# Optimization experiments

Measured on AMD Instinct MI355X. Metric: run time of the kernel, lower is better.

The kernel has to match this reference:

```python
import jax, jax.numpy as jnp
import numpy as np

VOCAB, EMBED, HIDDEN, NUM_CLASSES = 32000, 512, 1024, 10
PAD_IDX = 0


def setup_inputs() -> dict:
    key = jax.random.key(0)
    ks = jax.random.split(key, 8)
    x = jax.random.randint(ks[0], (64, 512), 0, VOCAB, dtype=jnp.int32)
    emb = jax.random.uniform(ks[1], (VOCAB, EMBED), jnp.float32, -0.1, 0.1)
    emb = emb.at[PAD_IDX].set(0.0)
    def xavier(k, shape):
        fan_out, fan_in = shape
        lim = jnp.sqrt(6.0 / (fan_in + fan_out)).astype(jnp.float32)
        return jax.random.uniform(k, shape, jnp.float32, -lim, lim)
    # layer 0: input EMBED+HIDDEN -> 4*HIDDEN; layer 1: 2*HIDDEN -> 4*HIDDEN
    W0 = xavier(ks[2], (4 * HIDDEN, EMBED + HIDDEN))
    W1 = xavier(ks[3], (4 * HIDDEN, 2 * HIDDEN))
    # bias: forget-gate chunk initialized to 1.0 (chunk order: i, f, g, o)
    b = jnp.zeros((4 * HIDDEN,), jnp.float32).at[HIDDEN:2 * HIDDEN].set(1.0)
    V = xavier(ks[4], (NUM_CLASSES, HIDDEN))
    bV = jnp.zeros((NUM_CLASSES,), jnp.float32)
    return {"x": x, "emb": emb, "W0": W0, "b0": b, "W1": W1, "b1": b, "V": V, "bV": bV}


def _cell(x_in, h, c, W, b):
    # gates: [B, 4H] = cat(x_in, h) @ W.T + b
    gates = jnp.concatenate([x_in, h], axis=-1) @ W.T + b
    i, f, g, o = jnp.split(gates, 4, axis=-1)
    c_new = jax.nn.sigmoid(f) * c + jax.nn.sigmoid(i) * jnp.tanh(g)
    h_new = jax.nn.sigmoid(o) * jnp.tanh(c_new)
    return h_new, c_new


def reference(x, emb, W0, b0, W1, b1, V, bV):
    B, T = x.shape
    embedded = emb[x]                       # [B, T, E]
    xs = jnp.swapaxes(embedded, 0, 1)       # [T, B, E]
    Ws, bs = (W0, W1), (b0, b1)
    h0 = jnp.zeros((2, B, HIDDEN), embedded.dtype)
    c0 = jnp.zeros((2, B, HIDDEN), embedded.dtype)

    def step(carry, x_t):
        h, c = carry
        layer_in = x_t
        hs, cs = [], []
        for i in range(2):
            h_new, c_new = _cell(layer_in, h[i], c[i], Ws[i], bs[i])
            hs.append(h_new)
            cs.append(c_new)
            layer_in = h_new
        return (jnp.stack(hs), jnp.stack(cs)), None

    (h_final, _), _ = jax.lax.scan(step, (h0, c0), xs)
    return h_final[-1] @ V.T + bV           # [B, NUM_CLASSES]
```

## Files before the change

### kernel.cpp

```cpp
#include <hip/hip_runtime.h>
#include <stdint.h>


typedef __attribute__((ext_vector_type(8))) short bf16x8;
typedef __attribute__((ext_vector_type(4))) float f32x4;

__device__ __forceinline__ unsigned short f2bf(float x) {
    unsigned u = __float_as_uint(x);
    u = (u + 0x7FFFu + ((u >> 16) & 1u)) >> 16;
    return (unsigned short)u;
}

__device__ __forceinline__ f32x4 mfma16(bf16x8 a, bf16x8 b, f32x4 c) {
    return __builtin_amdgcn_mfma_f32_16x16x32_bf16(a, b, c, 0, 0, 0);
}

__device__ __forceinline__ bf16x8 ldh(const unsigned short* p) {
    union { unsigned long long q[2]; bf16x8 v; } u;
    unsigned long long* a = (unsigned long long*)p;
    u.q[0] = __hip_atomic_load(a + 0, __ATOMIC_RELAXED, __HIP_MEMORY_SCOPE_AGENT);
    u.q[1] = __hip_atomic_load(a + 1, __ATOMIC_RELAXED, __HIP_MEMORY_SCOPE_AGENT);
    return u.v;
}

__device__ __forceinline__ void poll64(const unsigned int* base, int lane,
                                       unsigned target) {
    const unsigned int* p = base + lane;
    for (;;) {
        unsigned a = __hip_atomic_load(p, __ATOMIC_RELAXED, __HIP_MEMORY_SCOPE_AGENT);
        if (__all((int)(a >= target))) break;
        __builtin_amdgcn_s_sleep(2);
    }
}

__device__ __forceinline__ void poll128(const unsigned int* base, int lane,
                                        unsigned target) {
    const unsigned int* p0 = base + lane;
    const unsigned int* p1 = base + 64 + lane;
    for (;;) {
        unsigned a = __hip_atomic_load(p0, __ATOMIC_RELAXED, __HIP_MEMORY_SCOPE_AGENT);
        unsigned b = __hip_atomic_load(p1, __ATOMIC_RELAXED, __HIP_MEMORY_SCOPE_AGENT);
        if (__all((int)((a >= target) && (b >= target)))) break;
        __builtin_amdgcn_s_sleep(2);
    }
}

__device__ __forceinline__ float fsigm(float x) {
    x = fminf(fmaxf(x, -60.f), 60.f);
    return __builtin_amdgcn_rcpf(1.f + __expf(-x));
}
__device__ __forceinline__ float ftanh(float x) {
    x = fminf(fmaxf(x, -15.f), 15.f);
    float e = __expf(-2.f * x);
    return (1.f - e) * __builtin_amdgcn_rcpf(1.f + e);
}

__global__ __launch_bounds__(256) void embed_kernel(
    const int* __restrict__ x, const float* __restrict__ emb,
    unsigned short* __restrict__ xs)
{
    int e = blockIdx.x * 256 + threadIdx.x;
    int t  = e >> 12;
    int r  = e & 4095;
    int b  = r >> 6;
    int k8 = (r & 63) << 3;
    int tok = x[b * 512 + t];
    const float* src = emb + (size_t)tok * 512 + k8;
    unsigned short* dst = xs + ((size_t)(t * 64 + b)) * 512 + k8;
#pragma unroll
    for (int i = 0; i < 8; ++i) dst[i] = f2bf(src[i]);
}

__global__ __launch_bounds__(256) void init_kernel(unsigned int* __restrict__ p, int n)
{
    int i = blockIdx.x * 256 + threadIdx.x;
    if (i < n) p[i] = 0u;
}

#define LDS_GWS_OFF 131072
#define GWS_TILE    272
#define LDS_TOTAL   148480
#define RELIDX      2048
#define RING_MASK   127
#define SLOT_USH    65536
#define NBANK       16

__global__ __launch_bounds__(512) void lstm_kernel_df(
    const unsigned short* __restrict__ xs,
    unsigned short* __restrict__ h0ring,
    unsigned short* __restrict__ h1ring,
    float* __restrict__ h1f,
    unsigned int* __restrict__ bar,
    const float* __restrict__ W0, const float* __restrict__ b0,
    const float* __restrict__ W1, const float* __restrict__ b1)
{
    extern __shared__ char smem[];
    bf16x8* Afrag = (bf16x8*)smem;
    float*  gws   = (float*)(smem + LDS_GWS_OFF);

    const int wg  = blockIdx.x;
    const int tid = threadIdx.x;
    const bool isL1 = (wg >= 128);
    const int rr  = wg & 127;
    const int g   = rr >> 6;
    const int w   = rr & 63;
    const int w16 = w * 16;
    const float* W = isL1 ? W1 : W0;
    const int wstride = isL1 ? 2048 : 1536;
    const float* bias = isL1 ? b1 : b0;
    const unsigned int* bk = bar + (wg & (NBANK - 1)) * 256;

    for (int f = tid; f < 8192; f += 512) {
        int laneE = f & 63;
        int gt    = (f >> 6) & 3;
        int kb    = f >> 8;
        int m16   = laneE & 15;
        int q     = laneE >> 4;
        int c     = m16 >> 2;
        int s     = m16 & 3;
        int grow  = c * 1024 + w16 + gt * 4 + s;
        const float* src = W + (size_t)grow * wstride + kb * 32 + q * 8;
        bf16x8 v;
#pragma unroll
        for (int i = 0; i < 8; ++i) v[i] = (short)f2bf(src[i]);
        Afrag[f] = v;
    }

    const int lane = tid & 63;
    const int wid  = tid >> 6;
    const int bt   = wid & 1;
    const int ksh  = wid >> 1;
    const int n16  = lane & 15;
    const int q4   = lane >> 4;
    const int row  = g * 32 + bt * 16 + n16;
    const int nkreg = isL1 ? 8 : 4;

    bf16x8 rf[8][4];
    {
        int m16 = lane & 15;
        int q   = lane >> 4;
        int c   = m16 >> 2;
        int s   = m16 & 3;
#pragma unroll
        for (int jr = 0; jr < 8; ++jr) {
            if (jr < nkreg) {
                int kb = 32 + ksh + 4 * jr;
#pragma unroll
                for (int gt = 0; gt < 4; ++gt) {
                    int grow = c * 1024 + w16 + gt * 4 + s;
                    const float* src = W + (size_t)grow * wstride + kb * 32 + q * 8;
                    bf16x8 v;
#pragma unroll
                    for (int i = 0; i < 8; ++i) v[i] = (short)f2bf(src[i]);
                    rf[jr][gt] = v;
                }
            }
        }
    }

    const int eb   = tid >> 4;
    const int ecol = tid & 15;
    const int ebt  = tid >> 8;
    const int en   = eb & 15;
    const int egt  = ecol >> 2;
    const int es   = ecol & 3;
    const int erow = g * 32 + eb;
    float bi[4];
#pragma unroll
    for (int c = 0; c < 4; ++c) bi[c] = bias[c * 1024 + w16 + ecol];
    float cst = 0.f;
    const float* gs0 = gws + (size_t)((ebt * 2 + 0) * 4 + egt) * GWS_TILE + es * 17 + en;
    const float* gs1 = gws + (size_t)((ebt * 2 + 1) * 4 + egt) * GWS_TILE + es * 17 + en;
    float* gwr = gws + (size_t)((bt * 2 + (ksh & 1)) * 4) * GWS_TILE + q4 * 68 + n16;

    __syncthreads();

    f32x4 acc[4];
#pragma unroll
    for (int i = 0; i < 4; ++i) acc[i] = (f32x4){0.f, 0.f, 0.f, 0.f};

    if (!isL1) {
        const unsigned short* xsp = xs + ((size_t)row) * 512 + q4 * 8;
#pragma unroll
        for (int j = 0; j < 4; ++j) {
            int kb = ksh + 4 * j;
            bf16x8 bf = *(const bf16x8*)(xsp + kb * 32);
#pragma unroll
            for (int gt = 0; gt < 4; ++gt)
                acc[gt] = mfma16(Afrag[(kb * 4 + gt) * 64 + lane], bf, acc[gt]);
        }
    }

    for (int tick = 0; tick < 513; ++tick) {
        if (tick > 0) {
            unsigned target = (unsigned)tick;
            if ((tick & RING_MASK) == 0) {
                if (wid == 0)      poll128(bk,       lane, target);
                else if (wid == 4) poll128(bk + 128, lane, target);
                __syncthreads();
                if (wid == 0)
                    __builtin_amdgcn_fence(__ATOMIC_ACQUIRE, "agent");
                __syncthreads();
            } else {
                if (wid == 0)              poll64(bk + g * 64, lane, target);
                else if (isL1 && wid == 4) poll64(bk + 128 + g * 64, lane, target);
                __syncthreads();
            }
        }

        int t = isL1 ? (tick - 1) : tick;
        if (t >= 0 && t < 512) {
            if (!isL1) {
                if (t > 0) {
                    const unsigned short* hp =
                        h0ring + (size_t)((t - 1) & RING_MASK) * SLOT_USH
                               + (size_t)row * 1024 + q4 * 8;
#pragma unroll
                    for (int j = 4; j < 8; ++j) {
                        int kb = ksh + 4 * j;
                        bf16x8 bf = *(const bf16x8*)(hp + (kb - 16) * 32);
#pragma unroll
                        for (int gt = 0; gt < 4; ++gt)
                            acc[gt] = mfma16(Afrag[(kb * 4 + gt) * 64 + lane], bf, acc[gt]);
                    }
#pragma unroll
                    for (int j = 0; j < 4; ++j) {
                        int kb = 32 + ksh + 4 * j;
                        bf16x8 bf = *(const bf16x8*)(hp + (kb - 16) * 32);
#pragma unroll
                        for (int gt = 0; gt < 4; ++gt)
                            acc[gt] = mfma16(rf[j][gt], bf, acc[gt]);
                    }
                }
            } else {
                const unsigned short* hp0 =
                    h0ring + (size_t)(t & RING_MASK) * SLOT_USH
                           + (size_t)row * 1024 + q4 * 8;
#pragma unroll
                for (int j = 0; j < 8; ++j) {
                    int kb = ksh + 4 * j;
                    bf16x8 bf = *(const bf16x8*)(hp0 + kb * 32);
#pragma unroll
                    for (int gt = 0; gt < 4; ++gt)
                        acc[gt] = mfma16(Afrag[(kb * 4 + gt) * 64 + lane], bf, acc[gt]);
                }
                if (t > 0) {
                    const unsigned short* hp1 =
                        h1ring + (size_t)((t - 1) & RING_MASK) * SLOT_USH
                               + (size_t)row * 1024 + q4 * 8;
#pragma unroll
                    for (int j = 0; j < 8; ++j) {
                        int kb = ksh + 4 * j;
                        bf16x8 bf = *(const bf16x8*)(hp1 + kb * 32);
#pragma unroll
                        for (int gt = 0; gt < 4; ++gt)
                            acc[gt] = mfma16(rf[j][gt], bf, acc[gt]);
                    }
                }
            }

            if (ksh < 2) {
#pragma unroll
                for (int gt = 0; gt < 4; ++gt)
#pragma unroll
                    for (int r2 = 0; r2 < 4; ++r2)
                        gwr[gt * GWS_TILE + r2 * 17] = acc[gt][r2];
            }
            __syncthreads();
            if (ksh >= 2) {
#pragma unroll
                for (int gt = 0; gt < 4; ++gt)
#pragma unroll
                    for (int r2 = 0; r2 < 4; ++r2)
                        gwr[gt * GWS_TILE + r2 * 17] += acc[gt][r2];
            }
            __syncthreads();

            float xi = gs0[0]   + gs1[0]   + bi[0];
            float xf = gs0[68]  + gs1[68]  + bi[1];
            float xg = gs0[136] + gs1[136] + bi[2];
            float xo = gs0[204] + gs1[204] + bi[3];
            float si = fsigm(xi);
            float sf = fsigm(xf);
            float tg = ftanh(xg);
            float so = fsigm(xo);
            float cn = sf * cst + si * tg;
            cst = cn;
            float h  = so * ftanh(cn);
            unsigned hb  = (unsigned)f2bf(h);
            unsigned hup = (unsigned)__shfl_down((int)hb, 1);
            if (!(tid & 1)) {
                unsigned hv = hb | (hup << 16);
                unsigned short* hw =
                    (isL1 ? h1ring : h0ring) + (size_t)(t & RING_MASK) * SLOT_USH;
                unsigned int* hp32 =
                    (unsigned int*)(hw + (size_t)erow * 1024 + w16 + ecol);
                __hip_atomic_store(hp32, hv, __ATOMIC_RELAXED, __HIP_MEMORY_SCOPE_AGENT);
            }
            if (isL1 && t == 511)
                h1f[(size_t)erow * 1024 + w16 + ecol] = h;
            __syncthreads();
        }

        if (tick < 512) {
            if (tid < NBANK) {
                __hip_atomic_store(bar + tid * 256 + (isL1 ? 128 : 0) + g * 64 + w,
                                   (unsigned)(tick + 1),
                                   __ATOMIC_RELAXED, __HIP_MEMORY_SCOPE_AGENT);
            }
#pragma unroll
            for (int i = 0; i < 4; ++i) acc[i] = (f32x4){0.f, 0.f, 0.f, 0.f};
            int tn = tick + 1;
            if (!isL1 && tn < 512) {
                const unsigned short* xsp =
                    xs + ((size_t)(tn * 64 + row)) * 512 + q4 * 8;
#pragma unroll
                for (int j = 0; j < 4; ++j) {
                    int kb = ksh + 4 * j;
                    bf16x8 bf = *(const bf16x8*)(xsp + kb * 32);
#pragma unroll
                    for (int gt = 0; gt < 4; ++gt)
                        acc[gt] = mfma16(Afrag[(kb * 4 + gt) * 64 + lane], bf, acc[gt]);
                }
            }
        }
    }
}

__global__ __launch_bounds__(512) void lstm_kernel_fb(
    const unsigned short* __restrict__ xs,
    unsigned short* __restrict__ h0buf,
    unsigned short* __restrict__ h1buf,
    float* __restrict__ h1f,
    unsigned int* __restrict__ bar,
    const float* __restrict__ W0, const float* __restrict__ b0,
    const float* __restrict__ W1, const float* __restrict__ b1)
{
    extern __shared__ char smem[];
    bf16x8* Afrag = (bf16x8*)smem;
    float*  gws   = (float*)(smem + LDS_GWS_OFF);

    const int wg  = blockIdx.x;
    const int tid = threadIdx.x;
    const bool isL1 = (wg >= 128);
    const int w   = isL1 ? wg - 128 : wg;
    const int w8  = w * 8;
    const int nk  = isL1 ? 64 : 48;
    const float* W = isL1 ? W1 : W0;
    const int wstride = isL1 ? 2048 : 1536;
    const float* bias = isL1 ? b1 : b0;

    for (int f = tid; f < nk * 128; f += 512) {
        int kblk = f >> 7;
        int r    = f & 127;
        int mt   = r >> 6;
        int lane = r & 63;
        int m16  = lane & 15;
        int q    = lane >> 4;
        int c    = m16 >> 2;
        int ul   = mt * 4 + (m16 & 3);
        int grow = c * 1024 + w8 + ul;
        const float* src = W + (size_t)grow * wstride + kblk * 32 + q * 8;
        bf16x8 v;
#pragma unroll
        for (int i = 0; i < 8; ++i) v[i] = (short)f2bf(src[i]);
        Afrag[f] = v;
    }

    const int lane = tid & 63;
    const int wid  = tid >> 6;
    const int wv   = wid & 3;
    const int kh   = tid >> 8;
    const int n16  = lane & 15;
    const int q4   = lane >> 4;
    const int brow = wv * 16 + n16;

    float bi[2][4];
#pragma unroll
    for (int cell = 0; cell < 2; ++cell) {
        int j = w8 + q4 * 2 + cell;
#pragma unroll
        for (int c = 0; c < 4; ++c) bi[cell][c] = bias[c * 1024 + j];
    }
    float cst0 = 0.f, cst1 = 0.f;

    __syncthreads();

    f32x4 acc0 = (f32x4){0.f, 0.f, 0.f, 0.f};
    f32x4 acc1 = (f32x4){0.f, 0.f, 0.f, 0.f};

    if (!isL1) {
        const unsigned short* xsp = xs + ((size_t)brow) * 512 + q4 * 8;
        int k0 = kh ? 8 : 0;
#pragma unroll
        for (int kb2 = 0; kb2 < 8; ++kb2) {
            int kb = k0 + kb2;
            bf16x8 bf = *(const bf16x8*)(xsp + kb * 32);
            acc0 = mfma16(Afrag[(kb * 2 + 0) * 64 + lane], bf, acc0);
            acc1 = mfma16(Afrag[(kb * 2 + 1) * 64 + lane], bf, acc1);
        }
    }

    for (int tick = 0; tick < 513; ++tick) {
        if (tick > 0) {
            unsigned target = (unsigned)tick;
            if (wg == 0) {
                if (tid < 256) {
                    while (__hip_atomic_load(&bar[tid * 8], __ATOMIC_RELAXED,
                                             __HIP_MEMORY_SCOPE_AGENT) < target)
                        __builtin_amdgcn_s_sleep(1);
                }
                __syncthreads();
                if (tid < 8)
                    __hip_atomic_store(&bar[RELIDX + tid * 32], target,
                                       __ATOMIC_RELAXED, __HIP_MEMORY_SCOPE_AGENT);
            } else {
                if (tid == 0) {
                    while (__hip_atomic_load(&bar[RELIDX + (wg & 7) * 32],
                                             __ATOMIC_RELAXED,
                                             __HIP_MEMORY_SCOPE_AGENT) < target)
                        __builtin_amdgcn_s_sleep(1);
                }
                __syncthreads();
            }
            asm volatile("" ::: "memory");
        }

        int t = isL1 ? (tick - 1) : tick;
        if (t >= 0 && t < 512) {
            const int p = t & 1;

            if (!isL1) {
                const unsigned short* hp =
                    h0buf + (size_t)(p ^ 1) * 65536 + (size_t)brow * 1024 + q4 * 8;
                int k0 = kh ? 32 : 16;
#pragma unroll 8
                for (int kb2 = 0; kb2 < 16; ++kb2) {
                    int kb = k0 + kb2;
                    bf16x8 bf = ldh(hp + (kb - 16) * 32);
                    acc0 = mfma16(Afrag[(kb * 2 + 0) * 64 + lane], bf, acc0);
                    acc1 = mfma16(Afrag[(kb * 2 + 1) * 64 + lane], bf, acc1);
                }
            } else if (kh == 0) {
                const unsigned short* hp0 =
                    h0buf + (size_t)p * 65536 + (size_t)brow * 1024 + q4 * 8;
#pragma unroll 8
                for (int kb = 0; kb < 32; ++kb) {
                    bf16x8 bf = ldh(hp0 + kb * 32);
                    acc0 = mfma16(Afrag[(kb * 2 + 0) * 64 + lane], bf, acc0);
                    acc1 = mfma16(Afrag[(kb * 2 + 1) * 64 + lane], bf, acc1);
                }
            } else {
                const unsigned short* hp1 =
                    h1buf + (size_t)(p ^ 1) * 65536 + (size_t)brow * 1024 + q4 * 8;
#pragma unroll 8
                for (int kb = 32; kb < 64; ++kb) {
                    bf16x8 bf = ldh(hp1 + (kb - 32) * 32);
                    acc0 = mfma16(Afrag[(kb * 2 + 0) * 64 + lane], bf, acc0);
                    acc1 = mfma16(Afrag[(kb * 2 + 1) * 64 + lane], bf, acc1);
                }
            }

            float* gq = gws + wid * 512;
#pragma unroll
            for (int r = 0; r < 4; ++r) {
                gq[      q4 * 64 + r * 16 + n16] = acc0[r];
                gq[256 + q4 * 64 + r * 16 + n16] = acc1[r];
            }
            __syncthreads();

            if (kh == 0) {
                unsigned short* hw = (isL1 ? h1buf : h0buf) + (size_t)p * 65536;
                unsigned short hbits[2];
                float hflt[2];
#pragma unroll
                for (int cell = 0; cell < 2; ++cell) {
                    int ul = q4 * 2 + cell;
                    int mt = ul >> 2;
                    int r  = ul & 3;
                    const float* g0 = gws + wv * 512 + mt * 256;
                    const float* g1 = gws + (wv + 4) * 512 + mt * 256;
                    float xi = g0[0 * 64 + r * 16 + n16] + g1[0 * 64 + r * 16 + n16] + bi[cell][0];
                    float xf = g0[1 * 64 + r * 16 + n16] + g1[1 * 64 + r * 16 + n16] + bi[cell][1];
                    float xg = g0[2 * 64 + r * 16 + n16] + g1[2 * 64 + r * 16 + n16] + bi[cell][2];
                    float xo = g0[3 * 64 + r * 16 + n16] + g1[3 * 64 + r * 16 + n16] + bi[cell][3];
                    float si = fsigm(xi);
                    float sf = fsigm(xf);
                    float tg = ftanh(xg);
                    float so = fsigm(xo);
                    float cprev = cell ? cst1 : cst0;
                    float cn = sf * cprev + si * tg;
                    if (cell) cst1 = cn; else cst0 = cn;
                    float h = so * ftanh(cn);
                    hflt[cell]  = h;
                    hbits[cell] = f2bf(h);
                }
                unsigned int hv = (unsigned)hbits[0] | ((unsigned)hbits[1] << 16);
                unsigned int* hp32 =
                    (unsigned int*)(hw + (size_t)brow * 1024 + w8 + q4 * 2);
                __hip_atomic_store(hp32, hv, __ATOMIC_RELAXED, __HIP_MEMORY_SCOPE_AGENT);
                if (isL1 && t == 511) {
                    h1f[(size_t)brow * 1024 + w8 + q4 * 2 + 0] = hflt[0];
                    h1f[(size_t)brow * 1024 + w8 + q4 * 2 + 1] = hflt[1];
                }
            }
            __syncthreads();
        }

        if (tick < 512) {
            if (tid == 0) {
                asm volatile("s_waitcnt vmcnt(0)" ::: "memory");
                __hip_atomic_store(&bar[wg * 8], (unsigned)(tick + 1),
                                   __ATOMIC_RELAXED, __HIP_MEMORY_SCOPE_AGENT);
            }
            acc0 = (f32x4){0.f, 0.f, 0.f, 0.f};
            acc1 = (f32x4){0.f, 0.f, 0.f, 0.f};
            int tn = tick + 1;
            if (!isL1 && tn < 512) {
                const unsigned short* xsp =
                    xs + ((size_t)(tn * 64 + brow)) * 512 + q4 * 8;
                int k0 = kh ? 8 : 0;
#pragma unroll
                for (int kb2 = 0; kb2 < 8; ++kb2) {
                    int kb = k0 + kb2;
                    bf16x8 bf = *(const bf16x8*)(xsp + kb * 32);
                    acc0 = mfma16(Afrag[(kb * 2 + 0) * 64 + lane], bf, acc0);
                    acc1 = mfma16(Afrag[(kb * 2 + 1) * 64 + lane], bf, acc1);
                }
            }
        }
    }
}

__global__ __launch_bounds__(64) void cls_kernel(
    const float* __restrict__ h1f, const float* __restrict__ V,
    const float* __restrict__ bV, float* __restrict__ out)
{
    int b = blockIdx.x;
    int lane = threadIdx.x;
    float p[10];
#pragma unroll
    for (int c = 0; c < 10; ++c) p[c] = 0.f;
    for (int k = lane; k < 1024; k += 64) {
        float h = h1f[(size_t)b * 1024 + k];
#pragma unroll
        for (int c = 0; c < 10; ++c) p[c] += h * V[(size_t)c * 1024 + k];
    }
#pragma unroll
    for (int c = 0; c < 10; ++c) {
        float v = p[c];
#pragma unroll
        for (int off = 32; off > 0; off >>= 1) v += __shfl_down(v, off);
        if (lane == 0) out[b * 10 + c] = v + bV[c];
    }
}

extern "C" void kernel_launch(void* const* d_in, const int* in_sizes, int n_in,
                              void* d_out, int out_size, void* d_ws, size_t ws_size,
                              hipStream_t stream)
{
    const int*   x   = (const int*)d_in[0];
    const float* emb = (const float*)d_in[1];
    const float* W0  = (const float*)d_in[2];
    const float* b0  = (const float*)d_in[3];
    const float* W1  = (const float*)d_in[4];
    const float* b1  = (const float*)d_in[5];
    const float* V   = (const float*)d_in[6];
    const float* bV  = (const float*)d_in[7];
    float* out = (float*)d_out;

    char* ws = (char*)d_ws;
    unsigned short* xs = (unsigned short*)ws;

    if (ws_size >= 67387392ULL) {
        unsigned short* h0r = (unsigned short*)(ws + 33554432);
        unsigned short* h1r = (unsigned short*)(ws + 50331648);
        float*          h1f = (float*)(ws + 67108864);
        unsigned int*   bar = (unsigned int*)(ws + 67371008);

        hipLaunchKernelGGL(init_kernel, dim3(16), dim3(256), 0, stream,
                           bar, 4096);
        hipLaunchKernelGGL(embed_kernel, dim3(8192), dim3(256), 0, stream, x, emb, xs);
        hipLaunchKernelGGL(lstm_kernel_df, dim3(256), dim3(512), LDS_TOTAL, stream,
                           xs, h0r, h1r, h1f, bar, W0, b0, W1, b1);
        hipLaunchKernelGGL(cls_kernel, dim3(64), dim3(64), 0, stream, h1f, V, bV, out);
    } else {
        char* dyn = ws + 33554432;
        unsigned short* h0  = (unsigned short*)(dyn);
        unsigned short* h1  = (unsigned short*)(dyn + 262144);
        float*          h1f = (float*)(dyn + 524288);
        unsigned int*   bar = (unsigned int*)(dyn + 786432);

        hipLaunchKernelGGL(init_kernel, dim3(780), dim3(256), 0, stream,
                           (unsigned int*)dyn, 199680);
        hipLaunchKernelGGL(embed_kernel, dim3(8192), dim3(256), 0, stream, x, emb, xs);
        hipLaunchKernelGGL(lstm_kernel_fb, dim3(256), dim3(512), LDS_TOTAL, stream,
                           xs, h0, h1, h1f, bar, W0, b0, W1, b1);
        hipLaunchKernelGGL(cls_kernel, dim3(64), dim3(64), 0, stream, h1f, V, bV, out);
    }
}
```

Baseline: 3.050 ms.

## Restructure LSTM into role-split workgroups with local batch groups and partial-sum pipelines

```diff
diff --git a/kernel.cpp b/kernel.cpp
--- a/kernel.cpp
+++ b/kernel.cpp
@@ -4,102 +4,131 @@
 
 typedef __attribute__((ext_vector_type(8))) short bf16x8;
 typedef __attribute__((ext_vector_type(4))) float f32x4;
-
-__device__ __forceinline__ unsigned short f2bf(float x) {
+typedef unsigned short ush;
+typedef unsigned int u32;
+
+__device__ __forceinline__ ush f2bf(float x) {
     unsigned u = __float_as_uint(x);
     u = (u + 0x7FFFu + ((u >> 16) & 1u)) >> 16;
-    return (unsigned short)u;
+    return (ush)u;
 }
 
 __device__ __forceinline__ f32x4 mfma16(bf16x8 a, bf16x8 b, f32x4 c) {
     return __builtin_amdgcn_mfma_f32_16x16x32_bf16(a, b, c, 0, 0, 0);
 }
 
-__device__ __forceinline__ bf16x8 ldh(const unsigned short* p) {
+__device__ __forceinline__ float fsigm(float x) {
+    x = fminf(fmaxf(x, -60.f), 60.f);
+    return __builtin_amdgcn_rcpf(1.f + __expf(-x));
+}
+__device__ __forceinline__ float ftanh(float x) {
+    x = fminf(fmaxf(x, -15.f), 15.f);
+    float e = __expf(-2.f * x);
+    return (1.f - e) * __builtin_amdgcn_rcpf(1.f + e);
+}
+
+__device__ __forceinline__ u32 aload(const u32* p) {
+    return __hip_atomic_load(p, __ATOMIC_RELAXED, __HIP_MEMORY_SCOPE_AGENT);
+}
+__device__ __forceinline__ void astore(u32* p, u32 v) {
+    __hip_atomic_store(p, v, __ATOMIC_RELAXED, __HIP_MEMORY_SCOPE_AGENT);
+}
+__device__ __forceinline__ float aloadf(const float* p) {
+    return __hip_atomic_load(p, __ATOMIC_RELAXED, __HIP_MEMORY_SCOPE_AGENT);
+}
+__device__ __forceinline__ void astoref(float* p, float v) {
+    __hip_atomic_store(p, v, __ATOMIC_RELAXED, __HIP_MEMORY_SCOPE_AGENT);
+}
+__device__ __forceinline__ bf16x8 ldh(const ush* p) {
     union { unsigned long long q[2]; bf16x8 v; } u;
     unsigned long long* a = (unsigned long long*)p;
     u.q[0] = __hip_atomic_load(a + 0, __ATOMIC_RELAXED, __HIP_MEMORY_SCOPE_AGENT);
     u.q[1] = __hip_atomic_load(a + 1, __ATOMIC_RELAXED, __HIP_MEMORY_SCOPE_AGENT);
     return u.v;
 }
-
-__device__ __forceinline__ void poll64(const unsigned int* base, int lane,
-                                       unsigned target) {
-    const unsigned int* p = base + lane;
+#define WAITVM0() do { asm volatile("s_waitcnt vmcnt(0)" ::: "memory"); \
+                       __builtin_amdgcn_sched_barrier(0); } while (0)
+#define L1INV()  do { asm volatile("buffer_inv" ::: "memory"); \
+                      __builtin_amdgcn_sched_barrier(0); } while (0)
+__device__ __forceinline__ void barlg() {
+    asm volatile("s_waitcnt lgkmcnt(0)\ns_barrier" ::: "memory");
+    __builtin_amdgcn_sched_barrier(0);
+}
+
+__device__ __forceinline__ void poll64(const u32* base, int lane, unsigned target) {
+    const u32* p = base + lane;
     for (;;) {
-        unsigned a = __hip_atomic_load(p, __ATOMIC_RELAXED, __HIP_MEMORY_SCOPE_AGENT);
+        unsigned a = aload(p);
         if (__all((int)(a >= target))) break;
         __builtin_amdgcn_s_sleep(2);
     }
 }
-
-__device__ __forceinline__ void poll128(const unsigned int* base, int lane,
-                                        unsigned target) {
-    const unsigned int* p0 = base + lane;
-    const unsigned int* p1 = base + 64 + lane;
+__device__ __forceinline__ void poll128(const u32* base, int lane, unsigned target) {
+    const u32* p0 = base + lane;
+    const u32* p1 = base + 64 + lane;
     for (;;) {
-        unsigned a = __hip_atomic_load(p0, __ATOMIC_RELAXED, __HIP_MEMORY_SCOPE_AGENT);
-        unsigned b = __hip_atomic_load(p1, __ATOMIC_RELAXED, __HIP_MEMORY_SCOPE_AGENT);
+        unsigned a = aload(p0);
+        unsigned b = aload(p1);
         if (__all((int)((a >= target) && (b >= target)))) break;
         __builtin_amdgcn_s_sleep(2);
     }
 }
 
-__device__ __forceinline__ float fsigm(float x) {
-    x = fminf(fmaxf(x, -60.f), 60.f);
-    return __builtin_amdgcn_rcpf(1.f + __expf(-x));
-}
-__device__ __forceinline__ float ftanh(float x) {
-    x = fminf(fmaxf(x, -15.f), 15.f);
-    float e = __expf(-2.f * x);
-    return (1.f - e) * __builtin_amdgcn_rcpf(1.f + e);
-}
-
 __global__ __launch_bounds__(256) void embed_kernel(
     const int* __restrict__ x, const float* __restrict__ emb,
-    unsigned short* __restrict__ xs)
+    ush* __restrict__ xs)
 {
     int e = blockIdx.x * 256 + threadIdx.x;
     int t  = e >> 12;
-    int r  = e & 4095;
-    int b  = r >> 6;
-    int k8 = (r & 63) << 3;
+    int rr = e & 4095;
+    int b  = rr >> 6;
+    int k8 = (rr & 63) << 3;
     int tok = x[b * 512 + t];
     const float* src = emb + (size_t)tok * 512 + k8;
-    unsigned short* dst = xs + ((size_t)(t * 64 + b)) * 512 + k8;
+    ush* dst = xs + ((size_t)(t * 64 + b)) * 512 + k8;
 #pragma unroll
     for (int i = 0; i < 8; ++i) dst[i] = f2bf(src[i]);
 }
 
-__global__ __launch_bounds__(256) void init_kernel(unsigned int* __restrict__ p, int n)
+__global__ __launch_bounds__(256) void init_kernel(u32* __restrict__ p, int n)
 {
     int i = blockIdx.x * 256 + threadIdx.x;
     if (i < n) p[i] = 0u;
 }
 
+#define SLOTH 32768
+#define SLOTP 131072
+#define OFF_H0G 33554432ULL
+#define OFF_H0L 37748736ULL
+#define OFF_H1L 39845888ULL
+#define OFF_XP  41943040ULL
+#define OFF_HP  50331648ULL
+#define OFF_FL  58720256ULL
+#define OFF_H1F 67108864ULL
+#define OFF_BAR 67371008ULL
+#define FL_LOC  0
+#define FL_GA   256
+#define FL_GB   320
+#define FL_GLB  384
+#define FL_GD   448
+#define FL_DISC 512
 #define LDS_GWS_OFF 131072
 #define GWS_TILE    272
-#define LDS_TOTAL   148480
 #define RELIDX      2048
 #define RING_MASK   127
 #define SLOT_USH    65536
 #define NBANK       16
-
-__global__ __launch_bounds__(512) void lstm_kernel_df(
-    const unsigned short* __restrict__ xs,
-    unsigned short* __restrict__ h0ring,
-    unsigned short* __restrict__ h1ring,
-    float* __restrict__ h1f,
-    unsigned int* __restrict__ bar,
-    const float* __restrict__ W0, const float* __restrict__ b0,
-    const float* __restrict__ W1, const float* __restrict__ b1)
+#define LDS_LOCAL_TOTAL 151616
+#define LDS_FB_TOTAL    148480
+
+__device__ void fallback_df(char* smem, const ush* xs,
+    ush* h0ring, ush* h1ring, float* h1f, u32* bar,
+    const float* W0, const float* b0, const float* W1, const float* b1,
+    int wg, int tid)
 {
-    extern __shared__ char smem[];
     bf16x8* Afrag = (bf16x8*)smem;
     float*  gws   = (float*)(smem + LDS_GWS_OFF);
 
-    const int wg  = blockIdx.x;
-    const int tid = threadIdx.x;
     const bool isL1 = (wg >= 128);
     const int rr  = wg & 127;
     const int g   = rr >> 6;
@@ -108,7 +137,7 @@
     const float* W = isL1 ? W1 : W0;
     const int wstride = isL1 ? 2048 : 1536;
     const float* bias = isL1 ? b1 : b0;
-    const unsigned int* bk = bar + (wg & (NBANK - 1)) * 256;
+    const u32* bk = bar + (wg & (NBANK - 1)) * 256;
 
     for (int f = tid; f < 8192; f += 512) {
         int laneE = f & 63;
@@ -135,7 +164,7 @@
     const int row  = g * 32 + bt * 16 + n16;
     const int nkreg = isL1 ? 8 : 4;
 
-    bf16x8 rf[8][4];
+    bf16x8 rfb[8][4];
     {
         int m16 = lane & 15;
         int q   = lane >> 4;
@@ -152,7 +181,7 @@
                     bf16x8 v;
 #pragma unroll
                     for (int i = 0; i < 8; ++i) v[i] = (short)f2bf(src[i]);
-                    rf[jr][gt] = v;
+                    rfb[jr][gt] = v;
                 }
             }
         }
@@ -180,7 +209,7 @@
     for (int i = 0; i < 4; ++i) acc[i] = (f32x4){0.f, 0.f, 0.f, 0.f};
 
     if (!isL1) {
-        const unsigned short* xsp = xs + ((size_t)row) * 512 + q4 * 8;
+        const ush* xsp = xs + ((size_t)row) * 512 + q4 * 8;
 #pragma unroll
         for (int j = 0; j < 4; ++j) {
             int kb = ksh + 4 * j;
@@ -212,7 +241,7 @@
         if (t >= 0 && t < 512) {
             if (!isL1) {
                 if (t > 0) {
-                    const unsigned short* hp =
+                    const ush* hp =
                         h0ring + (size_t)((t - 1) & RING_MASK) * SLOT_USH
                                + (size_t)row * 1024 + q4 * 8;
 #pragma unroll
@@ -229,11 +258,11 @@
                         bf16x8 bf = *(const bf16x8*)(hp + (kb - 16) * 32);
 #pragma unroll
                         for (int gt = 0; gt < 4; ++gt)
-                            acc[gt] = mfma16(rf[j][gt], bf, acc[gt]);
+                            acc[gt] = mfma16(rfb[j][gt], bf, acc[gt]);
                     }
                 }
             } else {
-                const unsigned short* hp0 =
+                const ush* hp0 =
                     h0ring + (size_t)(t & RING_MASK) * SLOT_USH
                            + (size_t)row * 1024 + q4 * 8;
 #pragma unroll
@@ -245,7 +274,7 @@
                         acc[gt] = mfma16(Afrag[(kb * 4 + gt) * 64 + lane], bf, acc[gt]);
                 }
                 if (t > 0) {
-                    const unsigned short* hp1 =
+                    const ush* hp1 =
                         h1ring + (size_t)((t - 1) & RING_MASK) * SLOT_USH
                                + (size_t)row * 1024 + q4 * 8;
 #pragma unroll
@@ -254,7 +283,7 @@
                         bf16x8 bf = *(const bf16x8*)(hp1 + kb * 32);
 #pragma unroll
                         for (int gt = 0; gt < 4; ++gt)
-                            acc[gt] = mfma16(rf[j][gt], bf, acc[gt]);
+                            acc[gt] = mfma16(rfb[j][gt], bf, acc[gt]);
                     }
                 }
             }
@@ -291,11 +320,9 @@
             unsigned hup = (unsigned)__shfl_down((int)hb, 1);
             if (!(tid & 1)) {
                 unsigned hv = hb | (hup << 16);
-                unsigned short* hw =
-                    (isL1 ? h1ring : h0ring) + (size_t)(t & RING_MASK) * SLOT_USH;
-                unsigned int* hp32 =
-                    (unsigned int*)(hw + (size_t)erow * 1024 + w16 + ecol);
-                __hip_atomic_store(hp32, hv, __ATOMIC_RELAXED, __HIP_MEMORY_SCOPE_AGENT);
+                ush* hw = (isL1 ? h1ring : h0ring) + (size_t)(t & RING_MASK) * SLOT_USH;
+                u32* hp32 = (u32*)(hw + (size_t)erow * 1024 + w16 + ecol);
+                astore(hp32, hv);
             }
             if (isL1 && t == 511)
                 h1f[(size_t)erow * 1024 + w16 + ecol] = h;
@@ -304,16 +331,14 @@
 
         if (tick < 512) {
             if (tid < NBANK) {
-                __hip_atomic_store(bar + tid * 256 + (isL1 ? 128 : 0) + g * 64 + w,
-                                   (unsigned)(tick + 1),
-                                   __ATOMIC_RELAXED, __HIP_MEMORY_SCOPE_AGENT);
+                astore(bar + tid * 256 + (isL1 ? 128 : 0) + g * 64 + w,
+                       (unsigned)(tick + 1));
             }
 #pragma unroll
             for (int i = 0; i < 4; ++i) acc[i] = (f32x4){0.f, 0.f, 0.f, 0.f};
             int tn = tick + 1;
             if (!isL1 && tn < 512) {
-                const unsigned short* xsp =
-                    xs + ((size_t)(tn * 64 + row)) * 512 + q4 * 8;
+                const ush* xsp = xs + ((size_t)(tn * 64 + row)) * 512 + q4 * 8;
 #pragma unroll
                 for (int j = 0; j < 4; ++j) {
                     int kb = ksh + 4 * j;
@@ -327,12 +352,363 @@
     }
 }
 
+__device__ void run_local(char* smem, char* ws, const ush* xs,
+    const float* W0, const float* b0, const float* W1, const float* b1,
+    int wg, int tid)
+{
+    const int c   = wg & 7;
+    const int r   = wg >> 3;
+    const int rid = c >> 1;
+    const int g   = c & 1;
+    const int w32 = r * 32;
+
+    const float* W   = (rid == 0 || rid == 2) ? W0 : W1;
+    const int  wst   = (rid == 0 || rid == 2) ? 1536 : 2048;
+    const int  kofs  = (rid == 0) ? 512 : (rid == 1) ? 1024 : 0;
+
+    bf16x8* Afrag = (bf16x8*)smem;
+    float*  gws   = (float*)(smem + 131072);
+
+    ush* h0g = (ush*)(ws + OFF_H0G) + (size_t)g * 32 * SLOTH;
+    ush* h0l = (ush*)(ws + OFF_H0L) + (size_t)g * 16 * SLOTH;
+    ush* h1l = (ush*)(ws + OFF_H1L) + (size_t)g * 16 * SLOTH;
+    float* xpart = (float*)(ws + OFF_XP) + (size_t)g * 8 * SLOTP;
+    float* hpart = (float*)(ws + OFF_HP) + (size_t)g * 8 * SLOTP;
+    float* h1f   = (float*)(ws + OFF_H1F);
+    u32*   FL    = (u32*)(ws + OFF_FL);
+
+    for (int f = tid; f < 8192; f += 512) {
+        int laneE = f & 63;
+        int gt    = (f >> 6) & 7;
+        int kb    = f >> 9;
+        int m16   = laneE & 15;
+        int q     = laneE >> 4;
+        int cA    = m16 >> 2;
+        int sA    = m16 & 3;
+        int grow  = cA * 1024 + w32 + gt * 4 + sA;
+        const float* src = W + (size_t)grow * wst + kofs + kb * 32 + q * 8;
+        bf16x8 v;
+#pragma unroll
+        for (int i = 0; i < 8; ++i) v[i] = (short)f2bf(src[i]);
+        Afrag[f] = v;
+    }
+
+    const int lane = tid & 63;
+    const int wid  = tid >> 6;
+    const int bt   = wid & 1;
+    const int kq   = wid >> 1;
+    const int n16  = lane & 15;
+    const int q4   = lane >> 4;
+    const int rowL = bt * 16 + n16;
+
+    bf16x8 rf[4][8];
+    if (rid != 2) {
+        int m16 = lane & 15, q = lane >> 4;
+        int cA = m16 >> 2, sA = m16 & 3;
+#pragma unroll
+        for (int jr = 0; jr < 4; ++jr) {
+            int kb = 16 + kq + 4 * jr;
+#pragma unroll
+            for (int gt = 0; gt < 8; ++gt) {
+                int grow = cA * 1024 + w32 + gt * 4 + sA;
+                const float* src = W + (size_t)grow * wst + kofs + kb * 32 + q * 8;
+                bf16x8 v;
+#pragma unroll
+                for (int i = 0; i < 8; ++i) v[i] = (short)f2bf(src[i]);
+                rf[jr][gt] = v;
+            }
+        }
+    }
+
+    const int ecc = tid & 15;
+    const int b   = tid >> 4;
+    const int btE = b >> 4;
+    const int nE  = b & 15;
+    const bool evenT = !(tid & 1);
+
+    __syncthreads();
+
+    if (rid <= 1) {
+        ush* ringL = (rid == 0) ? h0l : h1l;
+        const float* part = (rid == 0) ? xpart : hpart;
+        u32* locfl  = FL + FL_LOC + c * 32;
+        u32* partfl = FL + ((rid == 0) ? FL_GB : FL_GLB) + g * 32 + r;
+        const float* bs = (rid == 0) ? b0 : b1;
+        float bi[2][4];
+#pragma unroll
+        for (int h = 0; h < 2; ++h)
+#pragma unroll
+            for (int cg = 0; cg < 4; ++cg)
+                bi[h][cg] = bs[cg * 1024 + w32 + ecc + 16 * h];
+        float cst[2] = {0.f, 0.f};
+
+        for (int t = 0; t < 512; ++t) {
+            if (wid == 0) {
+                const u32* pp; unsigned tgt;
+                if (lane < 32) { pp = locfl + lane; tgt = (unsigned)t; }
+                else           { pp = partfl; tgt = (lane == 32) ? (unsigned)(t + 1) : 0u; }
+                for (;;) {
+                    unsigned v = aload(pp);
+                    if (__all((int)(v >= tgt))) break;
+                    __builtin_amdgcn_s_sleep(2);
+                }
+            } else if (rid == 0 && wid == 1) {
+                const u32* pp = FL + FL_GLB + g * 32 + (lane & 31);
+                unsigned tgt = (t >= 26 && lane < 32) ? (unsigned)(t - 25) : 0u;
+                for (;;) {
+                    unsigned v = aload(pp);
+                    if (__all((int)(v >= tgt))) break;
+                    __builtin_amdgcn_s_sleep(2);
+                }
+            }
+            barlg();
+
+            bf16x8 B[8];
+            f32x4 acc[8];
+#pragma unroll
+            for (int i = 0; i < 8; ++i) acc[i] = (f32x4){0.f, 0.f, 0.f, 0.f};
+            if (t > 0) {
+                L1INV();
+                const ush* bp = ringL + (size_t)((t - 1) & 15) * SLOTH
+                              + (size_t)rowL * 1024 + q4 * 8;
+#pragma unroll
+                for (int j = 0; j < 8; ++j) B[j] = *(const bf16x8*)(bp + (kq + 4 * j) * 32);
+            }
+            float xp[8];
+            {
+                const float* pp = part + (size_t)(t & 7) * SLOTP + (size_t)b * 4096 + w32;
+#pragma unroll
+                for (int h = 0; h < 2; ++h)
+#pragma unroll
+                    for (int cg = 0; cg < 4; ++cg)
+                        xp[h * 4 + cg] = aloadf(pp + cg * 1024 + ecc + 16 * h);
+            }
+            if (t > 0) {
+#pragma unroll
+                for (int j = 0; j < 8; ++j) {
+                    int kb = kq + 4 * j;
+#pragma unroll
+                    for (int gt = 0; gt < 8; ++gt) {
+                        bf16x8 a = (j < 4) ? Afrag[(kb * 8 + gt) * 64 + lane] : rf[j - 4][gt];
+                        acc[gt] = mfma16(a, B[j], acc[gt]);
+                    }
+                }
+            }
+
+            u32 hvA = 0, hvB = 0;
+#pragma unroll
+            for (int h = 0; h < 2; ++h) {
+                if (kq < 2) {
+#pragma unroll
+                    for (int gt2 = 0; gt2 < 4; ++gt2)
+#pragma unroll
+                        for (int r2 = 0; r2 < 4; ++r2)
+                            gws[(size_t)((bt * 2 + kq) * 4 + gt2) * 321
+                                + (q4 * 4 + r2) * 20 + n16] = acc[h * 4 + gt2][r2];
+                }
+                barlg();
+                if (kq >= 2) {
+#pragma unroll
+                    for (int gt2 = 0; gt2 < 4; ++gt2)
+#pragma unroll
+                        for (int r2 = 0; r2 < 4; ++r2)
+                            gws[(size_t)((bt * 2 + (kq - 2)) * 4 + gt2) * 321
+                                + (q4 * 4 + r2) * 20 + n16] += acc[h * 4 + gt2][r2];
+                }
+                barlg();
+
+                int cc  = ecc + 16 * h;
+                int gt2 = (cc >> 2) & 3;
+                int s2  = cc & 3;
+                const float* g0 = gws + (size_t)((btE * 2 + 0) * 4 + gt2) * 321 + s2 * 20 + nE;
+                const float* g1 = gws + (size_t)((btE * 2 + 1) * 4 + gt2) * 321 + s2 * 20 + nE;
+                float xi = g0[0]   + g1[0]   + xp[h * 4 + 0] + bi[h][0];
+                float xf = g0[80]  + g1[80]  + xp[h * 4 + 1] + bi[h][1];
+                float xg = g0[160] + g1[160] + xp[h * 4 + 2] + bi[h][2];
+                float xo = g0[240] + g1[240] + xp[h * 4 + 3] + bi[h][3];
+                float si = fsigm(xi);
+                float sf = fsigm(xf);
+                float tg = ftanh(xg);
+                float so = fsigm(xo);
+                float cn = sf * cst[h] + si * tg;
+                cst[h] = cn;
+                float hval = so * ftanh(cn);
+                if (rid == 1 && t == 511)
+                    h1f[(size_t)(g * 32 + b) * 1024 + w32 + cc] = hval;
+                unsigned hb = (unsigned)f2bf(hval);
+                unsigned up = (unsigned)__shfl_down((int)hb, 1);
+                unsigned hv = hb | (up << 16);
+                if (h == 0) hvA = hv; else hvB = hv;
+                if (evenT) {
+                    u32* rs = (u32*)(ringL + (size_t)(t & 15) * SLOTH);
+                    astore(rs + ((b * 1024 + w32 + cc) >> 1), hv);
+                }
+                barlg();
+            }
+
+            WAITVM0();
+            barlg();
+            if (tid == 0)
+                astore(locfl + r, (u32)(t + 1));
+            if (rid == 0) {
+                if (tid == 64)
+                    astore(FL + FL_GA + g * 32 + r, (u32)t);
+                if (evenT) {
+                    u32* gp = (u32*)(h0g + (size_t)(t & 31) * SLOTH);
+                    int bi0 = (b * 1024 + w32 + ecc) >> 1;
+                    astore(gp + bi0,     hvA);
+                    astore(gp + bi0 + 8, hvB);
+                }
+            } else {
+                if (tid == 64)
+                    astore(FL + FL_GD + g * 32 + r, (u32)t);
+            }
+        }
+        WAITVM0();
+        if (tid == 64) {
+            u32* fin = FL + ((rid == 0) ? FL_GA : FL_GD) + g * 32 + r;
+            astore(fin, 512u);
+        }
+    } else {
+        float* ship  = (rid == 2) ? xpart : hpart;
+        u32* myflag  = FL + ((rid == 2) ? FL_GB : FL_GLB) + g * 32 + r;
+        u32* gA      = FL + FL_GA + g * 32;
+        u32* gD      = FL + FL_GD + g * 32;
+
+        for (int t = 0; t < 512; ++t) {
+            if (wid == 0) {
+                const u32* pp; unsigned tgt;
+                if (rid == 3) {
+                    pp  = (lane < 32) ? (gA + lane) : (gD + r);
+                    tgt = (lane < 32) ? (unsigned)(t + 1)
+                        : ((lane == 32 && t >= 7) ? (unsigned)(t - 6) : 0u);
+                } else {
+                    pp  = gA + r;
+                    tgt = (lane == 0 && t >= 7) ? (unsigned)(t - 6) : 0u;
+                }
+                for (;;) {
+                    unsigned v = aload(pp);
+                    if (__all((int)(v >= tgt))) break;
+                    __builtin_amdgcn_s_sleep(2);
+                }
+            }
+            WAITVM0();
+            barlg();
+            if (tid == 0 && t > 0)
+                astore(myflag, (u32)t);
+
+            f32x4 acc[8];
+#pragma unroll
+            for (int i = 0; i < 8; ++i) acc[i] = (f32x4){0.f, 0.f, 0.f, 0.f};
+            if (rid == 3) {
+                const ush* bp = h0g + (size_t)(t & 31) * SLOTH
+                              + (size_t)rowL * 1024 + q4 * 8;
+#pragma unroll
+                for (int j = 0; j < 8; ++j) {
+                    int kb = kq + 4 * j;
+                    bf16x8 bf = ldh(bp + kb * 32);
+#pragma unroll
+                    for (int gt = 0; gt < 8; ++gt) {
+                        bf16x8 a = (j < 4) ? Afrag[(kb * 8 + gt) * 64 + lane] : rf[j - 4][gt];
+                        acc[gt] = mfma16(a, bf, acc[gt]);
+                    }
+                }
+            } else {
+                const ush* bp = xs + (size_t)(t * 64 + g * 32 + rowL) * 512 + q4 * 8;
+#pragma unroll
+                for (int j = 0; j < 4; ++j) {
+                    int kb = kq + 4 * j;
+                    bf16x8 bf = *(const bf16x8*)(bp + kb * 32);
+#pragma unroll
+                    for (int gt = 0; gt < 8; ++gt)
+                        acc[gt] = mfma16(Afrag[(kb * 8 + gt) * 64 + lane], bf, acc[gt]);
+                }
+            }
+
+#pragma unroll
+            for (int h = 0; h < 2; ++h) {
+                if (kq < 2) {
+#pragma unroll
+                    for (int gt2 = 0; gt2 < 4; ++gt2)
+#pragma unroll
+                        for (int r2 = 0; r2 < 4; ++r2)
+                            gws[(size_t)((bt * 2 + kq) * 4 + gt2) * 321
+                                + (q4 * 4 + r2) * 20 + n16] = acc[h * 4 + gt2][r2];
+                }
+                barlg();
+                if (kq >= 2) {
+#pragma unroll
+                    for (int gt2 = 0; gt2 < 4; ++gt2)
+#pragma unroll
+                        for (int r2 = 0; r2 < 4; ++r2)
+                            gws[(size_t)((bt * 2 + (kq - 2)) * 4 + gt2) * 321
+                                + (q4 * 4 + r2) * 20 + n16] += acc[h * 4 + gt2][r2];
+                }
+                barlg();
+
+                int cc  = ecc + 16 * h;
+                int gt2 = (cc >> 2) & 3;
+                int s2  = cc & 3;
+                const float* g0 = gws + (size_t)((btE * 2 + 0) * 4 + gt2) * 321 + s2 * 20 + nE;
+                const float* g1 = gws + (size_t)((btE * 2 + 1) * 4 + gt2) * 321 + s2 * 20 + nE;
+                float* sp = ship + (size_t)(t & 7) * SLOTP + (size_t)b * 4096 + w32 + cc;
+                astoref(sp + 0,    g0[0]   + g1[0]);
+                astoref(sp + 1024, g0[80]  + g1[80]);
+                astoref(sp + 2048, g0[160] + g1[160]);
+                astoref(sp + 3072, g0[240] + g1[240]);
+                barlg();
+            }
+        }
+        WAITVM0();
+        if (tid == 0)
+            astore(myflag, 513u);
+    }
+}
+
+__global__ __launch_bounds__(512) void lstm_kernel_df(
+    const ush* __restrict__ xs, char* __restrict__ ws,
+    const float* __restrict__ W0, const float* __restrict__ b0,
+    const float* __restrict__ W1, const float* __restrict__ b1)
+{
+    extern __shared__ char smem[];
+    const int wg = blockIdx.x, tid = threadIdx.x;
+    __shared__ int s_mode;
+    u32* FL = (u32*)(ws + OFF_FL);
+
+    if (tid == 0) {
+        u32 xcc;
+        asm volatile("s_getreg_b32 %0, hwreg(HW_REG_XCC_ID)" : "=s"(xcc));
+        u32 ok = ((int)(xcc & 7) == (wg & 7)) ? 1u : 0u;
+        __hip_atomic_fetch_add(FL + FL_DISC, (1u << 9) | ok,
+                               __ATOMIC_RELAXED, __HIP_MEMORY_SCOPE_AGENT);
+        u32 v = 0; int it = 0;
+        for (;;) {
+            v = aload(FL + FL_DISC);
+            if ((v >> 9) >= 256) break;
+            if (++it > (1 << 20)) break;
+            __builtin_amdgcn_s_sleep(8);
+        }
+        s_mode = ((v & 511u) == 256u) ? 1 : 0;
+    }
+    __syncthreads();
+    const int mode = s_mode;
+
+    if (mode) {
+        run_local(smem, ws, xs, W0, b0, W1, b1, wg, tid);
+    } else {
+        fallback_df(smem, xs,
+                    (ush*)(ws + 33554432), (ush*)(ws + 50331648),
+                    (float*)(ws + OFF_H1F), (u32*)(ws + OFF_BAR),
+                    W0, b0, W1, b1, wg, tid);
+    }
+}
+
 __global__ __launch_bounds__(512) void lstm_kernel_fb(
-    const unsigned short* __restrict__ xs,
-    unsigned short* __restrict__ h0buf,
-    unsigned short* __restrict__ h1buf,
+    const ush* __restrict__ xs,
+    ush* __restrict__ h0buf,
+    ush* __restrict__ h1buf,
     float* __restrict__ h1f,
-    unsigned int* __restrict__ bar,
+    u32* __restrict__ bar,
     const float* __restrict__ W0, const float* __restrict__ b0,
     const float* __restrict__ W1, const float* __restrict__ b1)
 {
@@ -352,9 +728,9 @@
 
     for (int f = tid; f < nk * 128; f += 512) {
         int kblk = f >> 7;
-        int r    = f & 127;
-        int mt   = r >> 6;
-        int lane = r & 63;
+        int rr   = f & 127;
+        int mt   = rr >> 6;
+        int lane = rr & 63;
         int m16  = lane & 15;
         int q    = lane >> 4;
         int c    = m16 >> 2;
@@ -390,7 +766,7 @@
     f32x4 acc1 = (f32x4){0.f, 0.f, 0.f, 0.f};
 
     if (!isL1) {
-        const unsigned short* xsp = xs + ((size_t)brow) * 512 + q4 * 8;
+        const ush* xsp = xs + ((size_t)brow) * 512 + q4 * 8;
         int k0 = kh ? 8 : 0;
 #pragma unroll
         for (int kb2 = 0; kb2 < 8; ++kb2) {
@@ -406,19 +782,15 @@
             unsigned target = (unsigned)tick;
             if (wg == 0) {
                 if (tid < 256) {
-                    while (__hip_atomic_load(&bar[tid * 8], __ATOMIC_RELAXED,
-                                             __HIP_MEMORY_SCOPE_AGENT) < target)
+                    while (aload(&bar[tid * 8]) < target)
                         __builtin_amdgcn_s_sleep(1);
                 }
                 __syncthreads();
                 if (tid < 8)
-                    __hip_atomic_store(&bar[RELIDX + tid * 32], target,
-                                       __ATOMIC_RELAXED, __HIP_MEMORY_SCOPE_AGENT);
+                    astore(&bar[RELIDX + tid * 32], target);
             } else {
                 if (tid == 0) {
-                    while (__hip_atomic_load(&bar[RELIDX + (wg & 7) * 32],
-                                             __ATOMIC_RELAXED,
-                                             __HIP_MEMORY_SCOPE_AGENT) < target)
+                    while (aload(&bar[RELIDX + (wg & 7) * 32]) < target)
                         __builtin_amdgcn_s_sleep(1);
                 }
                 __syncthreads();
@@ -431,8 +803,7 @@
             const int p = t & 1;
 
             if (!isL1) {
-                const unsigned short* hp =
-                    h0buf + (size_t)(p ^ 1) * 65536 + (size_t)brow * 1024 + q4 * 8;
+                const ush* hp = h0buf + (size_t)(p ^ 1) * 65536 + (size_t)brow * 1024 + q4 * 8;
                 int k0 = kh ? 32 : 16;
 #pragma unroll 8
                 for (int kb2 = 0; kb2 < 16; ++kb2) {
@@ -442,8 +813,7 @@
                     acc1 = mfma16(Afrag[(kb * 2 + 1) * 64 + lane], bf, acc1);
                 }
             } else if (kh == 0) {
-                const unsigned short* hp0 =
-                    h0buf + (size_t)p * 65536 + (size_t)brow * 1024 + q4 * 8;
+                const ush* hp0 = h0buf + (size_t)p * 65536 + (size_t)brow * 1024 + q4 * 8;
 #pragma unroll 8
                 for (int kb = 0; kb < 32; ++kb) {
                     bf16x8 bf = ldh(hp0 + kb * 32);
@@ -451,8 +821,7 @@
                     acc1 = mfma16(Afrag[(kb * 2 + 1) * 64 + lane], bf, acc1);
                 }
             } else {
-                const unsigned short* hp1 =
-                    h1buf + (size_t)(p ^ 1) * 65536 + (size_t)brow * 1024 + q4 * 8;
+                const ush* hp1 = h1buf + (size_t)(p ^ 1) * 65536 + (size_t)brow * 1024 + q4 * 8;
 #pragma unroll 8
                 for (int kb = 32; kb < 64; ++kb) {
                     bf16x8 bf = ldh(hp1 + (kb - 32) * 32);
@@ -463,27 +832,27 @@
 
             float* gq = gws + wid * 512;
 #pragma unroll
-            for (int r = 0; r < 4; ++r) {
-                gq[      q4 * 64 + r * 16 + n16] = acc0[r];
-                gq[256 + q4 * 64 + r * 16 + n16] = acc1[r];
+            for (int rr = 0; rr < 4; ++rr) {
+                gq[      q4 * 64 + rr * 16 + n16] = acc0[rr];
+                gq[256 + q4 * 64 + rr * 16 + n16] = acc1[rr];
             }
             __syncthreads();
 
             if (kh == 0) {
-                unsigned short* hw = (isL1 ? h1buf : h0buf) + (size_t)p * 65536;
-                unsigned short hbits[2];
+                ush* hw = (isL1 ? h1buf : h0buf) + (size_t)p * 65536;
+                ush hbits[2];
                 float hflt[2];
 #pragma unroll
                 for (int cell = 0; cell < 2; ++cell) {
                     int ul = q4 * 2 + cell;
                     int mt = ul >> 2;
-                    int r  = ul & 3;
+                    int rr = ul & 3;
                     const float* g0 = gws + wv * 512 + mt * 256;
                     const float* g1 = gws + (wv + 4) * 512 + mt * 256;
-                    float xi = g0[0 * 64 + r * 16 + n16] + g1[0 * 64 + r * 16 + n16] + bi[cell][0];
-                    float xf = g0[1 * 64 + r * 16 + n16] + g1[1 * 64 + r * 16 + n16] + bi[cell][1];
-                    float xg = g0[2 * 64 + r * 16 + n16] + g1[2 * 64 + r * 16 + n16] + bi[cell][2];
-                    float xo = g0[3 * 64 + r * 16 + n16] + g1[3 * 64 + r * 16 + n16] + bi[cell][3];
+                    float xi = g0[0 * 64 + rr * 16 + n16] + g1[0 * 64 + rr * 16 + n16] + bi[cell][0];
+                    float xf = g0[1 * 64 + rr * 16 + n16] + g1[1 * 64 + rr * 16 + n16] + bi[cell][1];
+                    float xg = g0[2 * 64 + rr * 16 + n16] + g1[2 * 64 + rr * 16 + n16] + bi[cell][2];
+                    float xo = g0[3 * 64 + rr * 16 + n16] + g1[3 * 64 + rr * 16 + n16] + bi[cell][3];
                     float si = fsigm(xi);
                     float sf = fsigm(xf);
                     float tg = ftanh(xg);
@@ -495,10 +864,9 @@
                     hflt[cell]  = h;
                     hbits[cell] = f2bf(h);
                 }
-                unsigned int hv = (unsigned)hbits[0] | ((unsigned)hbits[1] << 16);
-                unsigned int* hp32 =
-                    (unsigned int*)(hw + (size_t)brow * 1024 + w8 + q4 * 2);
-                __hip_atomic_store(hp32, hv, __ATOMIC_RELAXED, __HIP_MEMORY_SCOPE_AGENT);
+                u32 hv = (u32)hbits[0] | ((u32)hbits[1] << 16);
+                u32* hp32 = (u32*)(hw + (size_t)brow * 1024 + w8 + q4 * 2);
+                astore(hp32, hv);
                 if (isL1 && t == 511) {
                     h1f[(size_t)brow * 1024 + w8 + q4 * 2 + 0] = hflt[0];
                     h1f[(size_t)brow * 1024 + w8 + q4 * 2 + 1] = hflt[1];
@@ -510,15 +878,13 @@
         if (tick < 512) {
             if (tid == 0) {
                 asm volatile("s_waitcnt vmcnt(0)" ::: "memory");
-                __hip_atomic_store(&bar[wg * 8], (unsigned)(tick + 1),
-                                   __ATOMIC_RELAXED, __HIP_MEMORY_SCOPE_AGENT);
+                astore(&bar[wg * 8], (unsigned)(tick + 1));
             }
             acc0 = (f32x4){0.f, 0.f, 0.f, 0.f};
             acc1 = (f32x4){0.f, 0.f, 0.f, 0.f};
             int tn = tick + 1;
             if (!isL1 && tn < 512) {
-                const unsigned short* xsp =
-                    xs + ((size_t)(tn * 64 + brow)) * 512 + q4 * 8;
+                const ush* xsp = xs + ((size_t)(tn * 64 + brow)) * 512 + q4 * 8;
                 int k0 = kh ? 8 : 0;
 #pragma unroll
                 for (int kb2 = 0; kb2 < 8; ++kb2) {
@@ -570,31 +936,30 @@
     float* out = (float*)d_out;
 
     char* ws = (char*)d_ws;
-    unsigned short* xs = (unsigned short*)ws;
+    ush* xs = (ush*)ws;
 
     if (ws_size >= 67387392ULL) {
-        unsigned short* h0r = (unsigned short*)(ws + 33554432);
-        unsigned short* h1r = (unsigned short*)(ws + 50331648);
-        float*          h1f = (float*)(ws + 67108864);
-        unsigned int*   bar = (unsigned int*)(ws + 67371008);
-
-        hipLaunchKernelGGL(init_kernel, dim3(16), dim3(256), 0, stream,
-                           bar, 4096);
+        float* h1f = (float*)(ws + OFF_H1F);
+        u32*   bar = (u32*)(ws + OFF_BAR);
+        u32*   fl  = (u32*)(ws + OFF_FL);
+
+        hipLaunchKernelGGL(init_kernel, dim3(16), dim3(256), 0, stream, bar, 4096);
+        hipLaunchKernelGGL(init_kernel, dim3(4),  dim3(256), 0, stream, fl, 1024);
         hipLaunchKernelGGL(embed_kernel, dim3(8192), dim3(256), 0, stream, x, emb, xs);
-        hipLaunchKernelGGL(lstm_kernel_df, dim3(256), dim3(512), LDS_TOTAL, stream,
-                           xs, h0r, h1r, h1f, bar, W0, b0, W1, b1);
+        hipLaunchKernelGGL(lstm_kernel_df, dim3(256), dim3(512), LDS_LOCAL_TOTAL, stream,
+                           xs, ws, W0, b0, W1, b1);
         hipLaunchKernelGGL(cls_kernel, dim3(64), dim3(64), 0, stream, h1f, V, bV, out);
     } else {
         char* dyn = ws + 33554432;
-        unsigned short* h0  = (unsigned short*)(dyn);
-        unsigned short* h1  = (unsigned short*)(dyn + 262144);
-        float*          h1f = (float*)(dyn + 524288);
-        unsigned int*   bar = (unsigned int*)(dyn + 786432);
+        ush*  h0  = (ush*)(dyn);
+        ush*  h1  = (ush*)(dyn + 262144);
+        float* h1f = (float*)(dyn + 524288);
+        u32*  bar = (u32*)(dyn + 786432);
 
         hipLaunchKernelGGL(init_kernel, dim3(780), dim3(256), 0, stream,
-                           (unsigned int*)dyn, 199680);
+                           (u32*)dyn, 199680);
         hipLaunchKernelGGL(embed_kernel, dim3(8192), dim3(256), 0, stream, x, emb, xs);
-        hipLaunchKernelGGL(lstm_kernel_fb, dim3(256), dim3(512), LDS_TOTAL, stream,
+        hipLaunchKernelGGL(lstm_kernel_fb, dim3(256), dim3(512), LDS_FB_TOTAL, stream,
                            xs, h0, h1, h1f, bar, W0, b0, W1, b1);
         hipLaunchKernelGGL(cls_kernel, dim3(64), dim3(64), 0, stream, h1f, V, bV, out);
     }
```

After: 5.733 ms. +88.0%, slower.
